# Kernel optimization log

Hardware: AMD Instinct MI355X
Metric: run time of the kernel (lower is better)

Reference implementation:

```python
import jax, jax.numpy as jnp
import numpy as np


def setup_inputs() -> dict:
    key = jax.random.key(0)
    ks = jax.random.split(key, 5)
    B, S, H, I, E = 4, 2048, 1024, 4096, 8
    scale_in = 1.0 / np.sqrt(H)
    scale_mid = 1.0 / np.sqrt(I)
    return {
        "x": jax.random.normal(ks[0], (B, S, H), dtype=jnp.float32),
        "w_gate": jax.random.normal(ks[1], (H, E), dtype=jnp.float32) * scale_in,
        "w1": jax.random.normal(ks[2], (E, H, I), dtype=jnp.float32) * scale_in,
        "w2": jax.random.normal(ks[3], (E, I, H), dtype=jnp.float32) * scale_mid,
        "w3": jax.random.normal(ks[4], (E, H, I), dtype=jnp.float32) * scale_in,
        "num_experts_per_tok": 2,
    }


def reference(x, w_gate, w1, w2, w3, num_experts_per_tok):
    """MoE with top-k routing and SwiGLU experts (Mixtral-style).

    x: [B, S, H]; w_gate: [H, E]; w1/w3: [E, H, I]; w2: [E, I, H].
    Returns [B, S, H]. Matches torch module output (aux_loss is a side
    attribute in the original, not returned).
    """
    B, S, H = x.shape
    E = w_gate.shape[1]
    K = num_experts_per_tok
    xf = x.reshape(-1, H)                           # [T, H]

    logits = xf @ w_gate                            # [T, E]
    probs = jax.nn.softmax(logits, axis=-1)
    topk_probs, topk_idx = jax.lax.top_k(probs, K)  # [T, K]
    topk_probs = topk_probs / topk_probs.sum(axis=-1, keepdims=True)

    # Per-token per-expert combine weight: sum over k of renormalized top-k
    # probs mapped back to expert slots. [T, E]
    comb = jnp.sum(jax.nn.one_hot(topk_idx, E, dtype=xf.dtype)
                   * topk_probs[..., None], axis=1)

    out = jnp.zeros_like(xf)
    for e in range(E):  # small fixed loop over experts
        hidden = jax.nn.silu(xf @ w1[e]) * (xf @ w3[e])  # [T, I]
        out = out + (hidden @ w2[e]) * comb[:, e:e + 1]
    return out.reshape(B, S, H)
```

## Files before the change

### kernel.cpp

```cpp
#include <hip/hip_runtime.h>

typedef unsigned short u16;
typedef __attribute__((ext_vector_type(4))) float f32x4;
typedef __attribute__((ext_vector_type(8))) short s16x8;

#define T_TOK 8192
#define HD    1024
#define ID    4096
#define NE    8
#define AK    (T_TOK * 2)
#define APAD  (AK + 256)
#define MTMAX 72

#define BAR()   __builtin_amdgcn_s_barrier()
#define SB0()   __builtin_amdgcn_sched_barrier(0)
#define PRIO1() __builtin_amdgcn_s_setprio(1)
#define PRIO0() __builtin_amdgcn_s_setprio(0)
#define WAITV6() asm volatile("s_waitcnt vmcnt(6)" ::: "memory")
#define WAITV8() asm volatile("s_waitcnt vmcnt(8)" ::: "memory")
#define LGKM0()  do { asm volatile("s_waitcnt lgkmcnt(0)" ::: "memory"); SB0(); } while (0)

__device__ __forceinline__ u16 f2bf(float f) {
  unsigned u = __builtin_bit_cast(unsigned, f);
  u += 0x7FFFu + ((u >> 16) & 1u);
  return (u16)(u >> 16);
}

__device__ __forceinline__ float bf2f(u16 v) {
  unsigned u = (unsigned)v << 16;
  return __builtin_bit_cast(float, u);
}

__device__ __forceinline__ void gld16(u16* lds, const u16* g) {
  __builtin_amdgcn_global_load_lds(
      (const __attribute__((address_space(1))) unsigned int*)g,
      (__attribute__((address_space(3))) unsigned int*)lds, 16, 0, 0);
}


__global__ void k_init(int* counts) {
  if (threadIdx.x < NE) counts[threadIdx.x] = 0;
}

__global__ void k_offsets(const int* __restrict__ counts, int* offs, int* cursors,
                          int* __restrict__ tiles, int* __restrict__ ntile) {
  if (threadIdx.x == 0) {
    int s = 0;
    for (int e = 0; e < NE; ++e) { offs[e] = s; s += counts[e]; }
    offs[NE] = s;
    int nt = 0;
    for (int e = 0; e < NE; ++e)
      for (int m0 = 0; m0 < counts[e]; m0 += 256)
        tiles[nt++] = (e << 16) | (m0 >> 8);
    ntile[0] = nt;
    for (int i = nt; i < MTMAX; ++i) tiles[i] = 0;
  }
  if (threadIdx.x < NE) cursors[threadIdx.x] = 0;
}

__global__ __launch_bounds__(256) void k_scatter(
    const int* __restrict__ tidx, const int* __restrict__ offs,
    int* cursors, int* __restrict__ list, int* __restrict__ pos) {
  int idx = blockIdx.x * 256 + threadIdx.x;
  if (idx >= AK) return;
  int e = tidx[idx];
  int p = atomicAdd(&cursors[e], 1);
  int a = offs[e] + p;
  list[a] = idx >> 1;
  pos[idx] = a;
}


#define NB_CVT 8192
#define NB_T13 16384
#define NB_T2  8192
#define NB_RTR 2048

__global__ __launch_bounds__(256) void k_prep(
    const float* __restrict__ x, const float* __restrict__ wg,
    const float* __restrict__ w1, const float* __restrict__ w2,
    const float* __restrict__ w3,
    u16* __restrict__ xb, u16* __restrict__ w13b, u16* __restrict__ w2b,
    int* __restrict__ tidx, float* __restrict__ tw, int* __restrict__ counts) {
  __shared__ char smem[32768];
  int bid = blockIdx.x, t = threadIdx.x;

  if (bid < NB_CVT) {
    int idx = bid * 256 + t;
    float4 v = ((const float4*)x)[idx];
    ushort4 o;
    o.x = f2bf(v.x); o.y = f2bf(v.y); o.z = f2bf(v.z); o.w = f2bf(v.w);
    ((ushort4*)xb)[idx] = o;
    return;
  }
  if (bid < NB_CVT + NB_T13) {
    u16 (*tile)[72] = (u16(*)[72])smem;
    int r = bid - NB_CVT;
    int bx = r & 63, by = (r >> 6) & 15, bz = r >> 10;
    int which = bz >> 3, e = bz & 7;
    const float* in = (which ? w3 : w1) + (size_t)e * HD * ID;
    int r0 = by * 64, c0 = bx * 64;
    int rr = t >> 4, cc = (t & 15) * 4;
#pragma unroll
    for (int i = 0; i < 4; ++i) {
      int rw = i * 16 + rr;
      float4 v = *(const float4*)&in[(size_t)(r0 + rw) * ID + c0 + cc];
      tile[cc + 0][rw] = f2bf(v.x);
      tile[cc + 1][rw] = f2bf(v.y);
      tile[cc + 2][rw] = f2bf(v.z);
      tile[cc + 3][rw] = f2bf(v.w);
    }
    __syncthreads();
    int c = t >> 3, ch = (t & 7) * 8;
#pragma unroll
    for (int j = 0; j < 2; ++j) {
      int crow = c0 + j * 32 + c;
      int pr = ((crow >> 4) << 5) + which * 16 + (crow & 15);
      *(s16x8*)&w13b[((size_t)e * 2 * ID + pr) * HD + r0 + ch] =
          *(const s16x8*)&tile[j * 32 + c][ch];
    }
    return;
  }
  if (bid < NB_CVT + NB_T13 + NB_T2) {
    u16 (*tile)[72] = (u16(*)[72])smem;
    int r = bid - NB_CVT - NB_T13;
    int bx = r & 15, by = (r >> 4) & 63, bz = r >> 10;
    const int R = ID, C = HD;
    size_t base = (size_t)bz * R * C;
    int r0 = by * 64, c0 = bx * 64;
    int rr = t >> 4, cc = (t & 15) * 4;
#pragma unroll
    for (int i = 0; i < 4; ++i) {
      int rw = i * 16 + rr;
      float4 v = *(const float4*)&w2[base + (size_t)(r0 + rw) * C + c0 + cc];
      tile[cc + 0][rw] = f2bf(v.x);
      tile[cc + 1][rw] = f2bf(v.y);
      tile[cc + 2][rw] = f2bf(v.z);
      tile[cc + 3][rw] = f2bf(v.w);
    }
    __syncthreads();
    int c = t >> 3, ch = (t & 7) * 8;
#pragma unroll
    for (int j = 0; j < 2; ++j) {
      int cr = j * 32 + c;
      *(s16x8*)&w2b[base + (size_t)(c0 + cr) * R + r0 + ch] =
          *(const s16x8*)&tile[cr][ch];
    }
    return;
  }
  {
    float* wgs = (float*)smem;
    int blockR = bid - NB_CVT - NB_T13 - NB_T2;
    for (int i = t; i < NE * HD; i += 256) {
      int h = i >> 3, e = i & 7;
      wgs[e * HD + h] = wg[i];
    }
    __syncthreads();
    int lane = t & 63, wid = t >> 6;
    int tok = blockR * 4 + wid;
    const float* xr = x + (size_t)tok * HD;
    double acc[NE];
#pragma unroll
    for (int e = 0; e < NE; ++e) acc[e] = 0.0;
    for (int i = 0; i < HD / 64; ++i) {
      float xv = xr[lane + i * 64];
#pragma unroll
      for (int e = 0; e < NE; ++e)
        acc[e] += (double)xv * (double)wgs[e * HD + lane + i * 64];
    }
#pragma unroll
    for (int e = 0; e < NE; ++e)
      for (int s = 32; s >= 1; s >>= 1) acc[e] += __shfl_xor(acc[e], s, 64);
    int e0 = 0; double m0 = acc[0];
    for (int e = 1; e < NE; ++e) if (acc[e] > m0) { m0 = acc[e]; e0 = e; }
    int e1 = -1; double m1 = -1e300;
    for (int e = 0; e < NE; ++e) if (e != e0 && acc[e] > m1) { m1 = acc[e]; e1 = e; }
    if (lane == 0) {
      double d = exp(m1 - m0);
      tidx[tok * 2] = e0; tidx[tok * 2 + 1] = e1;
      tw[tok * 2] = (float)(1.0 / (1.0 + d));
      tw[tok * 2 + 1] = (float)(d / (1.0 + d));
      atomicAdd(&counts[e0], 1);
      atomicAdd(&counts[e1], 1);
    }
  }
}


#define GEMM_CORE(NTK, NITER) \
  int wr = wid >> 2, wc = wid & 3; \
  int lane15 = lane & 15, lq = lane >> 4, sw8 = lane15 & 7; \
  f32x4 acc[8][4]; \
  _Pragma("unroll") for (int m = 0; m < 8; ++m) \
    _Pragma("unroll") for (int n = 0; n < 4; ++n) acc[m][n] = (f32x4){0.f,0.f,0.f,0.f}; \
  auto stgA = [&](int bb, int h, int kt) { \
    gld16(&As[bb][(h*128 + 0*64 + wid*8) * 64], gA[h*2+0] + kt*64); \
    gld16(&As[bb][(h*128 + 1*64 + wid*8) * 64], gA[h*2+1] + kt*64); }; \
  auto stgB = [&](int bb, int h, int kt) { \
    gld16(&Bs[bb][(h*128 + 0*64 + wid*8) * 64], gB[h*2+0] + kt*64); \
    gld16(&Bs[bb][(h*128 + 1*64 + wid*8) * 64], gB[h*2+1] + kt*64); }; \
  s16x8 a[4][2], b[4][2]; \
  auto rdA = [&](int bb, int mh) { \
    _Pragma("unroll") for (int mm = 0; mm < 4; ++mm) \
      _Pragma("unroll") for (int kk = 0; kk < 2; ++kk) \
        a[mm][kk] = *(const s16x8*)&As[bb][(mh*128 + wr*64 + mm*16 + lane15)*64 + (((kk*4+lq)^sw8)*8)]; }; \
  auto rdB = [&](int bb, int fh) { \
    _Pragma("unroll") for (int ff = 0; ff < 2; ++ff) \
      _Pragma("unroll") for (int kk = 0; kk < 2; ++kk) \
        b[fh*2+ff][kk] = *(const s16x8*)&Bs[bb][(fh*128 + wc*32 + ff*16 + lane15)*64 + (((kk*4+lq)^sw8)*8)]; }; \
  auto mf = [&](int mh, int fh) { \
    _Pragma("unroll") for (int mm = 0; mm < 4; ++mm) \
      _Pragma("unroll") for (int ff = 0; ff < 2; ++ff) { \
        acc[mh*4+mm][fh*2+ff] = __builtin_amdgcn_mfma_f32_16x16x32_bf16(a[mm][0], b[fh*2+ff][0], acc[mh*4+mm][fh*2+ff], 0, 0, 0); \
        acc[mh*4+mm][fh*2+ff] = __builtin_amdgcn_mfma_f32_16x16x32_bf16(a[mm][1], b[fh*2+ff][1], acc[mh*4+mm][fh*2+ff], 0, 0, 0); } }; \
   \
  stgA(0,0,0); stgB(0,0,0); stgA(0,1,0); stgB(0,1,0); stgA(1,0,1); stgB(1,0,1); \
  WAITV8(); BAR(); SB0(); \
  for (int i = 0; i < (NITER); ++i) { \
    int ku2 = (2*i+2) & ((NTK)-1), ku3 = (2*i+3) & ((NTK)-1); \
     rdA(0,0); rdB(0,0); stgA(1,1,2*i+1); WAITV6(); BAR(); LGKM0(); PRIO1(); mf(0,0); PRIO0(); BAR(); SB0(); \
     rdB(0,1); stgB(1,1,2*i+1); BAR(); LGKM0(); PRIO1(); mf(0,1); PRIO0(); BAR(); SB0(); \
     rdA(0,1); stgA(0,0,ku2); BAR(); LGKM0(); PRIO1(); mf(1,0); PRIO0(); BAR(); SB0(); \
     stgB(0,0,ku2); WAITV8(); BAR(); PRIO1(); mf(1,1); PRIO0(); BAR(); SB0(); \
     rdA(1,0); rdB(1,0); stgA(0,1,ku2); WAITV6(); BAR(); LGKM0(); PRIO1(); mf(0,0); PRIO0(); BAR(); SB0(); \
     rdB(1,1); stgB(0,1,ku2); BAR(); LGKM0(); PRIO1(); mf(0,1); PRIO0(); BAR(); SB0(); \
     rdA(1,1); stgA(1,0,ku3); BAR(); LGKM0(); PRIO1(); mf(1,0); PRIO0(); BAR(); SB0(); \
     stgB(1,0,ku3); WAITV8(); BAR(); PRIO1(); mf(1,1); PRIO0(); BAR(); SB0(); \
  }

__global__ __launch_bounds__(512, 1) void k_gemm1(
    const u16* __restrict__ xb, const u16* __restrict__ w13b,
    const int* __restrict__ list, const int* __restrict__ offs,
    const int* __restrict__ tiles, const int* __restrict__ ntile,
    u16* __restrict__ hidden) {
  int ti = blockIdx.y;
  if (ti >= ntile[0]) return;
  int packed = tiles[ti];
  int e = packed >> 16;
  int m0 = (packed & 0xFFFF) << 8;
  int aoff = offs[e];
  int cnt = offs[e + 1] - aoff;
  int n0 = blockIdx.x * 256;

  __shared__ u16 As[2][256 * 64];
  __shared__ u16 Bs[2][256 * 64];

  int tid = threadIdx.x, lane = tid & 63, wid = tid >> 6;
  int l8 = lane >> 3, c8 = lane & 7;
  int csrc = (c8 ^ l8) * 8;

  const u16* gA[4]; const u16* gB[4];
#pragma unroll
  for (int h = 0; h < 2; ++h)
#pragma unroll
    for (int c = 0; c < 2; ++c) {
      int row = h * 128 + c * 64 + wid * 8 + l8;
      int rr = m0 + row; if (rr > cnt - 1) rr = cnt - 1;
      gA[h*2+c] = xb + (size_t)list[aoff + rr] * HD + csrc;
      gB[h*2+c] = w13b + ((size_t)e * 2 * ID + n0 + row) * HD + csrc;
    }

  GEMM_CORE(HD / 64, HD / 128)

#pragma unroll
  for (int mh = 0; mh < 2; ++mh)
#pragma unroll
    for (int mm = 0; mm < 4; ++mm)
#pragma unroll
      for (int j = 0; j < 4; ++j) {
        int grow = m0 + mh * 128 + wr * 64 + mm * 16 + lq * 4 + j;
        if (grow < cnt) {
          size_t rbase = (size_t)(aoff + grow) * ID;
#pragma unroll
          for (int p = 0; p < 2; ++p) {
            float v1 = acc[mh*4+mm][2*p][j];
            float v3 = acc[mh*4+mm][2*p+1][j];
            float s = v1 / (1.0f + __expf(-v1));
            int icol = ((n0 + p * 128 + wc * 32) >> 1) + lane15;
            hidden[rbase + icol] = f2bf(s * v3);
          }
        }
      }
}

__global__ __launch_bounds__(512, 1) void k_gemm2(
    const u16* __restrict__ hidden, const u16* __restrict__ w2b,
    const int* __restrict__ offs, const int* __restrict__ tiles,
    const int* __restrict__ ntile,
    u16* __restrict__ yp0, u16* __restrict__ yp3) {
  int ti = blockIdx.y;
  if (ti >= ntile[0]) return;
  int packed = tiles[ti];
  int e = packed >> 16;
  int m0 = (packed & 0xFFFF) << 8;
  int aoff = offs[e];
  int cnt = offs[e + 1] - aoff;
  int n0 = (blockIdx.x & 3) * 256;
  int kidx = blockIdx.x >> 2;
  int kc = kidx * 1024;

  __shared__ u16 As[2][256 * 64];
  __shared__ u16 Bs[2][256 * 64];

  int tid = threadIdx.x, lane = tid & 63, wid = tid >> 6;
  int l8 = lane >> 3, c8 = lane & 7;
  int csrc = (c8 ^ l8) * 8;

  const u16* gA[4]; const u16* gB[4];
#pragma unroll
  for (int h = 0; h < 2; ++h)
#pragma unroll
    for (int c = 0; c < 2; ++c) {
      int row = h * 128 + c * 64 + wid * 8 + l8;
      gA[h*2+c] = hidden + (size_t)(aoff + m0 + row) * ID + kc + csrc;
      gB[h*2+c] = w2b + ((size_t)e * HD + n0 + row) * ID + kc + csrc;
    }

  GEMM_CORE(1024 / 64, 1024 / 128)

  u16* yp = (kidx < 3) ? yp0 + (size_t)kidx * AK * HD : yp3;
#pragma unroll
  for (int mh = 0; mh < 2; ++mh)
#pragma unroll
    for (int mm = 0; mm < 4; ++mm)
#pragma unroll
      for (int j = 0; j < 4; ++j) {
        int grow = m0 + mh * 128 + wr * 64 + mm * 16 + lq * 4 + j;
        if (grow < cnt) {
          u16* yrow = yp + (size_t)(aoff + grow) * HD;
#pragma unroll
          for (int f = 0; f < 4; ++f) {
            int col = n0 + (f >> 1) * 128 + wc * 32 + (f & 1) * 16 + lane15;
            yrow[col] = f2bf(acc[mh*4+mm][f][j]);
          }
        }
      }
}

__global__ __launch_bounds__(256) void k_combine(
    const u16* __restrict__ yp0, const u16* __restrict__ yp3,
    const int* __restrict__ pos, const float* __restrict__ tw,
    float* __restrict__ out) {
  int t = blockIdx.x;
  int c = threadIdx.x * 4;
  int a0 = pos[t * 2], a1 = pos[t * 2 + 1];
  float w0 = tw[t * 2], w1 = tw[t * 2 + 1];
  float s0[4] = {0.f, 0.f, 0.f, 0.f}, s1[4] = {0.f, 0.f, 0.f, 0.f};
#pragma unroll
  for (int k = 0; k < 4; ++k) {
    const u16* yp = (k < 3) ? yp0 + (size_t)k * AK * HD : yp3;
    ushort4 v0 = *(const ushort4*)&yp[(size_t)a0 * HD + c];
    ushort4 v1 = *(const ushort4*)&yp[(size_t)a1 * HD + c];
    s0[0] += bf2f(v0.x); s0[1] += bf2f(v0.y); s0[2] += bf2f(v0.z); s0[3] += bf2f(v0.w);
    s1[0] += bf2f(v1.x); s1[1] += bf2f(v1.y); s1[2] += bf2f(v1.z); s1[3] += bf2f(v1.w);
  }
  float4 o;
  o.x = w0 * s0[0] + w1 * s1[0];
  o.y = w0 * s0[1] + w1 * s1[1];
  o.z = w0 * s0[2] + w1 * s1[2];
  o.w = w0 * s0[3] + w1 * s1[3];
  *(float4*)&out[(size_t)t * HD + c] = o;
}


extern "C" void kernel_launch(void* const* d_in, const int* in_sizes, int n_in,
                              void* d_out, int out_size, void* d_ws, size_t ws_size,
                              hipStream_t stream) {
  const float* x  = (const float*)d_in[0];
  const float* wg = (const float*)d_in[1];
  const float* w1 = (const float*)d_in[2];
  const float* w2 = (const float*)d_in[3];
  const float* w3 = (const float*)d_in[4];

  char* p = (char*)d_ws;
  auto alloc = [&](size_t bytes) {
    char* r = p;
    p += (bytes + 255) & ~(size_t)255;
    return r;
  };
  u16*   xb      = (u16*)alloc((size_t)T_TOK * HD * 2);
  u16*   w13b    = (u16*)alloc((size_t)NE * 2 * ID * HD * 2);
  u16*   w2b     = (u16*)alloc((size_t)NE * HD * ID * 2);
  u16*   hidden  = (u16*)alloc((size_t)APAD * ID * 2);
  u16*   yp3     = (u16*)alloc((size_t)AK * HD * 2);
  int*   tidx    = (int*)alloc(AK * 4);
  float* tw      = (float*)alloc(AK * 4);
  int*   list    = (int*)alloc(AK * 4);
  int*   pos     = (int*)alloc(AK * 4);
  int*   counts  = (int*)alloc(64);
  int*   offs    = (int*)alloc(64);
  int*   cursors = (int*)alloc(64);
  int*   tiles   = (int*)alloc(MTMAX * 4);
  int*   ntile   = (int*)alloc(64);
  (void)ws_size; (void)in_sizes; (void)n_in; (void)out_size;

  u16* yp0 = w13b;

  k_init<<<1, 64, 0, stream>>>(counts);
  k_prep<<<NB_CVT + NB_T13 + NB_T2 + NB_RTR, 256, 0, stream>>>(
      x, wg, w1, w2, w3, xb, w13b, w2b, tidx, tw, counts);
  k_offsets<<<1, 64, 0, stream>>>(counts, offs, cursors, tiles, ntile);
  k_scatter<<<AK / 256, 256, 0, stream>>>(tidx, offs, cursors, list, pos);

  dim3 gg1(2 * ID / 256, MTMAX, 1);
  k_gemm1<<<gg1, 512, 0, stream>>>(xb, w13b, list, offs, tiles, ntile, hidden);
  dim3 gg2(16, MTMAX, 1);
  k_gemm2<<<gg2, 512, 0, stream>>>(hidden, w2b, offs, tiles, ntile, yp0, yp3);
  k_combine<<<T_TOK, 256, 0, stream>>>(yp0, yp3, pos, tw, (float*)d_out);
}
```

Before: 876.9 us.

## Restructure weight transpose-convert into larger swizzled tiles and split prep kernels

Replaces the 64x64 transpose-and-convert blocks with 256x64 tiles that use an XOR-swizzled LDS layout, and writes each output row as eight 16-byte stores per thread. The w2 conversion moves into its own kernel, and the x conversion now handles 8 elements per thread. The MFMA order inside the GEMM is also changed so the k index is the outer loop. The aim is to cut block count and launch overhead and to improve store coalescing in the prep phase, which moves a large amount of fp32 weight data. The cost is more work per block and higher LDS use, which lowers occupancy.

After: 915.9 us. 4.4% more time.

```diff
diff --git a/kernel.cpp b/kernel.cpp
--- a/kernel.cpp
+++ b/kernel.cpp
@@ -71,86 +71,75 @@
 }
 
 
-#define NB_CVT 8192
-#define NB_T13 16384
-#define NB_T2  8192
-#define NB_RTR 2048
-
-__global__ __launch_bounds__(256) void k_prep(
+__device__ __forceinline__ void tconv_block(
+    const float* __restrict__ in, u16* __restrict__ out,
+    int R, int C, int r0, int c0, int which, int interleave, char* smem) {
+  u16 (*tile)[264] = (u16(*)[264])smem;
+  int t = threadIdx.x;
+  int rr = t >> 4;
+  int cc4 = (t & 15) * 4;
+#pragma unroll
+  for (int i = 0; i < 16; ++i) {
+    int r = i * 16 + rr;
+    float4 v = *(const float4*)&in[(size_t)(r0 + r) * C + c0 + cc4];
+    u16 bv[4] = {f2bf(v.x), f2bf(v.y), f2bf(v.z), f2bf(v.w)};
+#pragma unroll
+    for (int q = 0; q < 4; ++q) {
+      int c = cc4 + q;
+      tile[c][(((r >> 3) ^ (c & 7)) << 3) | (r & 7)] = bv[q];
+    }
+  }
+  __syncthreads();
+  int c = t >> 2;
+  int ro = (t & 3) * 64;
+  int gc = c0 + c;
+  int orow = interleave ? (((gc >> 4) << 5) + which * 16 + (gc & 15)) : gc;
+  u16* obase = out + (size_t)orow * R + r0;
+#pragma unroll
+  for (int j = 0; j < 8; ++j) {
+    int roff = ro + j * 8;
+    int phys = (((roff >> 3) ^ (c & 7)) << 3);
+    *(s16x8*)&obase[roff] = *(const s16x8*)&tile[c][phys];
+  }
+}
+
+#define NBA_CVT 4096
+#define NBA_T13 4096
+
+__global__ __launch_bounds__(256) void k_prepA(
     const float* __restrict__ x, const float* __restrict__ wg,
-    const float* __restrict__ w1, const float* __restrict__ w2,
-    const float* __restrict__ w3,
-    u16* __restrict__ xb, u16* __restrict__ w13b, u16* __restrict__ w2b,
+    const float* __restrict__ w1, const float* __restrict__ w3,
+    u16* __restrict__ xb, u16* __restrict__ w13b,
     int* __restrict__ tidx, float* __restrict__ tw, int* __restrict__ counts) {
-  __shared__ char smem[32768];
+  __shared__ char smem[64 * 264 * 2];
   int bid = blockIdx.x, t = threadIdx.x;
 
-  if (bid < NB_CVT) {
+  if (bid < NBA_CVT) {
     int idx = bid * 256 + t;
-    float4 v = ((const float4*)x)[idx];
-    ushort4 o;
-    o.x = f2bf(v.x); o.y = f2bf(v.y); o.z = f2bf(v.z); o.w = f2bf(v.w);
-    ((ushort4*)xb)[idx] = o;
+    float4 v0 = ((const float4*)x)[idx * 2];
+    float4 v1 = ((const float4*)x)[idx * 2 + 1];
+    s16x8 o;
+    o[0] = (short)f2bf(v0.x); o[1] = (short)f2bf(v0.y);
+    o[2] = (short)f2bf(v0.z); o[3] = (short)f2bf(v0.w);
+    o[4] = (short)f2bf(v1.x); o[5] = (short)f2bf(v1.y);
+    o[6] = (short)f2bf(v1.z); o[7] = (short)f2bf(v1.w);
+    ((s16x8*)xb)[idx] = o;
     return;
   }
-  if (bid < NB_CVT + NB_T13) {
-    u16 (*tile)[72] = (u16(*)[72])smem;
-    int r = bid - NB_CVT;
-    int bx = r & 63, by = (r >> 6) & 15, bz = r >> 10;
+  if (bid < NBA_CVT + NBA_T13) {
+    int r = bid - NBA_CVT;
+    int bx = r & 63;
+    int by = (r >> 6) & 3;
+    int bz = r >> 8;
     int which = bz >> 3, e = bz & 7;
     const float* in = (which ? w3 : w1) + (size_t)e * HD * ID;
-    int r0 = by * 64, c0 = bx * 64;
-    int rr = t >> 4, cc = (t & 15) * 4;
-#pragma unroll
-    for (int i = 0; i < 4; ++i) {
-      int rw = i * 16 + rr;
-      float4 v = *(const float4*)&in[(size_t)(r0 + rw) * ID + c0 + cc];
-      tile[cc + 0][rw] = f2bf(v.x);
-      tile[cc + 1][rw] = f2bf(v.y);
-      tile[cc + 2][rw] = f2bf(v.z);
-      tile[cc + 3][rw] = f2bf(v.w);
-    }
-    __syncthreads();
-    int c = t >> 3, ch = (t & 7) * 8;
-#pragma unroll
-    for (int j = 0; j < 2; ++j) {
-      int crow = c0 + j * 32 + c;
-      int pr = ((crow >> 4) << 5) + which * 16 + (crow & 15);
-      *(s16x8*)&w13b[((size_t)e * 2 * ID + pr) * HD + r0 + ch] =
-          *(const s16x8*)&tile[j * 32 + c][ch];
-    }
-    return;
-  }
-  if (bid < NB_CVT + NB_T13 + NB_T2) {
-    u16 (*tile)[72] = (u16(*)[72])smem;
-    int r = bid - NB_CVT - NB_T13;
-    int bx = r & 15, by = (r >> 4) & 63, bz = r >> 10;
-    const int R = ID, C = HD;
-    size_t base = (size_t)bz * R * C;
-    int r0 = by * 64, c0 = bx * 64;
-    int rr = t >> 4, cc = (t & 15) * 4;
-#pragma unroll
-    for (int i = 0; i < 4; ++i) {
-      int rw = i * 16 + rr;
-      float4 v = *(const float4*)&w2[base + (size_t)(r0 + rw) * C + c0 + cc];
-      tile[cc + 0][rw] = f2bf(v.x);
-      tile[cc + 1][rw] = f2bf(v.y);
-      tile[cc + 2][rw] = f2bf(v.z);
-      tile[cc + 3][rw] = f2bf(v.w);
-    }
-    __syncthreads();
-    int c = t >> 3, ch = (t & 7) * 8;
-#pragma unroll
-    for (int j = 0; j < 2; ++j) {
-      int cr = j * 32 + c;
-      *(s16x8*)&w2b[base + (size_t)(c0 + cr) * R + r0 + ch] =
-          *(const s16x8*)&tile[cr][ch];
-    }
+    tconv_block(in, w13b + (size_t)e * 2 * ID * HD,
+                HD, ID, by * 256, bx * 64, which, 1, smem);
     return;
   }
   {
     float* wgs = (float*)smem;
-    int blockR = bid - NB_CVT - NB_T13 - NB_T2;
+    int blockR = bid - NBA_CVT - NBA_T13;
     for (int i = t; i < NE * HD; i += 256) {
       int h = i >> 3, e = i & 7;
       wgs[e * HD + h] = wg[i];
@@ -184,6 +173,17 @@
       atomicAdd(&counts[e1], 1);
     }
   }
+}
+
+__global__ __launch_bounds__(256) void k_prepB(
+    const float* __restrict__ w2, u16* __restrict__ w2b) {
+  __shared__ char smem[64 * 264 * 2];
+  int bid = blockIdx.x;
+  int bx = bid & 15;
+  int by = (bid >> 4) & 15;
+  int e = bid >> 8;
+  tconv_block(w2 + (size_t)e * ID * HD, w2b + (size_t)e * HD * ID,
+              ID, HD, by * 256, bx * 64, 0, 0, smem);
 }
 
 
@@ -209,10 +209,10 @@
       _Pragma("unroll") for (int kk = 0; kk < 2; ++kk) \
         b[fh*2+ff][kk] = *(const s16x8*)&Bs[bb][(fh*128 + wc*32 + ff*16 + lane15)*64 + (((kk*4+lq)^sw8)*8)]; }; \
   auto mf = [&](int mh, int fh) { \
-    _Pragma("unroll") for (int mm = 0; mm < 4; ++mm) \
-      _Pragma("unroll") for (int ff = 0; ff < 2; ++ff) { \
-        acc[mh*4+mm][fh*2+ff] = __builtin_amdgcn_mfma_f32_16x16x32_bf16(a[mm][0], b[fh*2+ff][0], acc[mh*4+mm][fh*2+ff], 0, 0, 0); \
-        acc[mh*4+mm][fh*2+ff] = __builtin_amdgcn_mfma_f32_16x16x32_bf16(a[mm][1], b[fh*2+ff][1], acc[mh*4+mm][fh*2+ff], 0, 0, 0); } }; \
+    _Pragma("unroll") for (int kk = 0; kk < 2; ++kk) \
+      _Pragma("unroll") for (int mm = 0; mm < 4; ++mm) \
+        _Pragma("unroll") for (int ff = 0; ff < 2; ++ff) \
+          acc[mh*4+mm][fh*2+ff] = __builtin_amdgcn_mfma_f32_16x16x32_bf16(a[mm][kk], b[fh*2+ff][kk], acc[mh*4+mm][fh*2+ff], 0, 0, 0); }; \
    \
   stgA(0,0,0); stgB(0,0,0); stgA(0,1,0); stgB(0,1,0); stgA(1,0,1); stgB(1,0,1); \
   WAITV8(); BAR(); SB0(); \
@@ -397,8 +397,9 @@
   u16* yp0 = w13b;
 
   k_init<<<1, 64, 0, stream>>>(counts);
-  k_prep<<<NB_CVT + NB_T13 + NB_T2 + NB_RTR, 256, 0, stream>>>(
-      x, wg, w1, w2, w3, xb, w13b, w2b, tidx, tw, counts);
+  k_prepA<<<NBA_CVT + NBA_T13 + 2048, 256, 0, stream>>>(
+      x, wg, w1, w3, xb, w13b, tidx, tw, counts);
+  k_prepB<<<2048, 256, 0, stream>>>(w2, w2b);
   k_offsets<<<1, 64, 0, stream>>>(counts, offs, cursors, tiles, ntile);
   k_scatter<<<AK / 256, 256, 0, stream>>>(tidx, offs, cursors, list, pos);
 
```
